# Optimization experiments

Hardware: AMD Instinct MI355X
Metric: run time of the kernel (lower is better)

## Reference

```python
import jax, jax.numpy as jnp
import numpy as np

N, E, IN_F, EDGE_F, HID, S = 200000, 600000, 28, 4, 128, 20000
NUM_LAYERS = 4
L = NUM_LAYERS - 1
BN_EPS = 1e-5


def setup_inputs() -> dict:
    key = jax.random.key(0)
    ks = jax.random.split(key, 20)
    p = lambda k, shape: (jax.random.normal(k, shape, dtype=jnp.float32) * 0.1)
    return {
        'x': jax.random.normal(ks[0], (N, IN_F), dtype=jnp.float32),
        'edge_index': jax.random.randint(ks[1], (2, E), 0, N),
        'edge_attr': jax.random.normal(ks[2], (E, EDGE_F), dtype=jnp.float32),
        'edge_weight': jax.random.uniform(ks[3], (E,), dtype=jnp.float32),
        'node_mask': (jax.random.uniform(ks[4], (N,)) > 0.5).astype(jnp.float32),
        'subgraphs2nodes': jax.random.randint(ks[5], (N,), 0, S),
        # layer-1 params (in_features -> hidden)
        'be1_W1': p(ks[6], (EDGE_F, IN_F)), 'be1_b1': jnp.zeros((IN_F,), jnp.float32),
        'be1_W2': p(ks[7], (IN_F, IN_F)), 'be1_b2': jnp.zeros((IN_F,), jnp.float32),
        'm1_W1': p(ks[8], (IN_F, HID)), 'm1_b1': jnp.zeros((HID,), jnp.float32),
        'm1_W2': p(ks[9], (HID, HID)), 'm1_b2': jnp.zeros((HID,), jnp.float32),
        'bn1_g': jnp.ones((HID,), jnp.float32), 'bn1_b': jnp.zeros((HID,), jnp.float32),
        'eps1': jnp.zeros((), jnp.float32),
        # layers 2..NUM_LAYERS, stacked (hidden -> hidden)
        'beW1': p(ks[10], (L, EDGE_F, HID)), 'beb1': jnp.zeros((L, HID), jnp.float32),
        'beW2': p(ks[11], (L, HID, HID)), 'beb2': jnp.zeros((L, HID), jnp.float32),
        'mW1': p(ks[12], (L, HID, HID)), 'mb1': jnp.zeros((L, HID), jnp.float32),
        'mW2': p(ks[13], (L, HID, HID)), 'mb2': jnp.zeros((L, HID), jnp.float32),
        'bng': jnp.ones((L, HID), jnp.float32), 'bnb': jnp.zeros((L, HID), jnp.float32),
        'eps': jnp.zeros((L,), jnp.float32),
    }


def _mlp2(h, W1, b1, W2, b2):
    # Linear -> ReLU -> Linear
    return jnp.dot(jax.nn.relu(jnp.dot(h, W1) + b1), W2) + b2


def _gine(x, src, dst, edge_attr, edge_weight, eps,
          beW1, beb1, beW2, beb2, W1, b1, W2, b2, g, beta):
    # bond encoder on edge features
    e = _mlp2(edge_attr, beW1, beb1, beW2, beb2)            # [E, d]
    # message: relu(x_j + e_ij) * w_ij, aggregated at dst via scatter-add
    m = jax.nn.relu(x[src] + e) * edge_weight[:, None]      # [E, d]
    aggr = jax.ops.segment_sum(m, dst, num_segments=N)      # [N, d]
    h = (1.0 + eps) * x + aggr
    # node MLP: Linear,ReLU,Linear,BN(train mode),ReLU
    h = _mlp2(h, W1, b1, W2, b2)
    mu = jnp.mean(h, axis=0)
    var = jnp.mean((h - mu) ** 2, axis=0)
    h = (h - mu) * jax.lax.rsqrt(var + BN_EPS) * g + beta
    return jax.nn.relu(h)


def reference(x, edge_index, edge_attr, edge_weight, node_mask, subgraphs2nodes,
              be1_W1, be1_b1, be1_W2, be1_b2, m1_W1, m1_b1, m1_W2, m1_b2,
              bn1_g, bn1_b, eps1,
              beW1, beb1, beW2, beb2, mW1, mb1, mW2, mb2, bng, bnb, eps):
    src, dst = edge_index[0], edge_index[1]
    h = _gine(x, src, dst, edge_attr, edge_weight, eps1,
              be1_W1, be1_b1, be1_W2, be1_b2,
              m1_W1, m1_b1, m1_W2, m1_b2, bn1_g, bn1_b)
    for i in range(L):
        h_new = _gine(h, src, dst, edge_attr, edge_weight, eps[i],
                      beW1[i], beb1[i], beW2[i], beb2[i],
                      mW1[i], mb1[i], mW2[i], mb2[i], bng[i], bnb[i])
        h = h + h_new  # residual
    # float node_mask branch + global_add_pool over subgraphs2nodes
    h = h * node_mask[:, None]
    return jax.ops.segment_sum(h, subgraphs2nodes, num_segments=S)  # [S, HID]
```

## Files before the change

kernel.cpp:

```cpp
#include <hip/hip_runtime.h>
#include <hip/hip_bf16.h>


#define BNEPS 1e-5f
#define LDA 136
#define SCAN_NB 240

typedef __attribute__((ext_vector_type(8))) short bf16x8;
typedef __attribute__((ext_vector_type(8))) unsigned short u16x8;
typedef __attribute__((ext_vector_type(4))) float f32x4;

__device__ inline short f2bf(float f) {
    __hip_bfloat16 h = __float2bfloat16(f);
    return *reinterpret_cast<short*>(&h);
}
__device__ inline unsigned short f2bfu(float f) {
    __hip_bfloat16 h = __float2bfloat16(f);
    return *reinterpret_cast<unsigned short*>(&h);
}
__device__ inline float bf2f(unsigned short u) {
    union { unsigned int i; float f; } v; v.i = ((unsigned int)u) << 16; return v.f;
}


// ... 245 lines not shown
    }
    if (tid < 32) b2s[tid] = (tid < 28) ? b2[tid] : 0.f;
    int j = tid & 31, sub = tid >> 5;
    float w10 = 0.f, w11 = 0.f, w12 = 0.f, w13 = 0.f, b1j = 0.f;
    if (j < 28) { w10 = W1[j]; w11 = W1[28 + j]; w12 = W1[56 + j]; w13 = W1[84 + j]; b1j = b1[j]; }
    int w = tid >> 6, lane = tid & 63;
    int l15 = lane & 15, quad = lane >> 4;
    __syncthreads();

    int numTiles = (E + 63) >> 6;
    for (int tile = blockIdx.x; tile < numTiles; tile += gridDim.x) {
        int base = tile * 64;
        __syncthreads();
        if (tid < 64) {
            int k = base + tid;
            float4 a = (k < E) ? pea4[k] : make_float4(0.f, 0.f, 0.f, 0.f);
            eas[tid][0] = a.x; eas[tid][1] = a.y; eas[tid][2] = a.z; eas[tid][3] = a.w;
        }
        __syncthreads();
        #pragma unroll
        for (int q = 0; q < 8; ++q) {
            int e = q * 8 + sub;
            float t = fmaf(eas[e][0], w10, fmaf(eas[e][1], w11,
                      fmaf(eas[e][2], w12, fmaf(eas[e][3], w13, b1j))));
            As[e * 40 + j] = (j < 28) ? f2bf(fmaxf(t, 0.f)) : (short)0;
        }
        __syncthreads();
        f32x4 acc[2];
        acc[0] = (f32x4){0.f, 0.f, 0.f, 0.f};
        acc[1] = (f32x4){0.f, 0.f, 0.f, 0.f};
        bf16x8 af = *(bf16x8*)&As[(w * 16 + l15) * 40 + quad * 8];
        #pragma unroll
        for (int nt = 0; nt < 2; ++nt) {
            bf16x8 bf = *(bf16x8*)&Bs[(nt * 16 + l15) * 40 + quad * 8];
            acc[nt] = __builtin_amdgcn_mfma_f32_16x16x32_bf16(af, bf, acc[nt], 0, 0, 0);
        }
        __syncthreads();
        #pragma unroll
        for (int nt = 0; nt < 2; ++nt) {
            int col = nt * 16 + l15;
            float bb = b2s[col];
            #pragma unroll
            for (int r = 0; r < 4; ++r)
                As[(w * 16 + quad * 4 + r) * 40 + col] = f2bf(acc[nt][r] + bb);
        }
        __syncthreads();
        for (int i = tid; i < 64 * 28; i += 256) {
            int row = i / 28, col = i - row * 28;
            int gr = base + row;
            if (gr < E) emsg28[(size_t)gr * 28 + col] = As[row * 40 + col];
        }
    }
}

__global__ __launch_bounds__(256) void k_gather(
    const unsigned short* __restrict__ h, const int* __restrict__ offs,
    const int2* __restrict__ pmeta, const unsigned short* __restrict__ emsg,
    unsigned short* __restrict__ a0,
    const float* __restrict__ epsp, int epsIdx,
    int n0, int n1)
{
    int grp = threadIdx.x >> 5, lane = threadIdx.x & 31;
    int n = n0 + blockIdx.x * 8 + grp;
    if (n >= n1) return;
    int e0 = offs[n0];
    int k0 = offs[n], k1 = offs[n + 1];
    float s = 1.0f + epsp[epsIdx];
    ushort4 hv0 = *(const ushort4*)&h[(size_t)n * 128 + lane * 4];
    float m0 = s * bf2f(hv0.x), m1 = s * bf2f(hv0.y);
    float m2 = s * bf2f(hv0.z), m3 = s * bf2f(hv0.w);
    int2 mtA, mtB, mtC, mtD;
    ushort4 evA, hvA, evB, hvB, evC, hvC, evD, hvD;
    const ushort4 z4 = {0, 0, 0, 0};
    #define GSLOT(mt, ev, hv, kk) \
        if ((kk) < k1) { \
            mt = pmeta[kk]; \
            ev = *(const ushort4*)&emsg[(size_t)((kk) - e0) * 128 + lane * 4]; \
            hv = *(const ushort4*)&h[(size_t)mt.x * 128 + lane * 4]; \
        } else { mt = make_int2(0, 0); ev = z4; hv = z4; }
    #define GCONS(mt, ev, hv) { \
            float wv = __int_as_float(mt.y); \
            m0 += fmaxf(bf2f(hv.x) + bf2f(ev.x), 0.f) * wv; \
            m1 += fmaxf(bf2f(hv.y) + bf2f(ev.y), 0.f) * wv; \
            m2 += fmaxf(bf2f(hv.z) + bf2f(ev.z), 0.f) * wv; \
            m3 += fmaxf(bf2f(hv.w) + bf2f(ev.w), 0.f) * wv; }
    GSLOT(mtA, evA, hvA, k0)
    GSLOT(mtB, evB, hvB, k0 + 1)
    GSLOT(mtC, evC, hvC, k0 + 2)
    GSLOT(mtD, evD, hvD, k0 + 3)
    int k = k0;
    while (true) {
        GCONS(mtA, evA, hvA)
        GCONS(mtB, evB, hvB)
        GCONS(mtC, evC, hvC)
        GCONS(mtD, evD, hvD)
        k += 4;
        if (k >= k1) break;
        GSLOT(mtA, evA, hvA, k)
        GSLOT(mtB, evB, hvB, k + 1)
        GSLOT(mtC, evC, hvC, k + 2)
        GSLOT(mtD, evD, hvD, k + 3)
    }
    #undef GSLOT
    #undef GCONS
    ushort4 o;
    o.x = f2bfu(m0); o.y = f2bfu(m1); o.z = f2bfu(m2); o.w = f2bfu(m3);
    *(ushort4*)&a0[(size_t)n * 128 + lane * 4] = o;
}

__global__ __launch_bounds__(256) void k_gather28(
    const float* __restrict__ x, const unsigned short* __restrict__ xbf,
    const int* __restrict__ offs,
    const int2* __restrict__ pmeta, const unsigned short* __restrict__ emsg28,
    const float* __restrict__ eps1, float* __restrict__ u28, int N)
{
    int grp = threadIdx.x >> 5, lane = threadIdx.x & 31;
    int n = blockIdx.x * 8 + grp;
    if (n >= N || lane >= 28) return;
    float s = 1.0f + eps1[0];
    int k0 = offs[n], k1 = offs[n + 1];
    float m = 0.f;
    int2 mtA, mtB, mtC, mtD;
    unsigned short eA, xA, eB, xB, eC, xC, eD, xD;
    #define GSLOT28(mt, ee, xx, kk) \
        if ((kk) < k1) { \
            mt = pmeta[kk]; \
            ee = emsg28[(size_t)(kk) * 28 + lane]; \
            xx = xbf[(size_t)mt.x * 32 + lane]; \
        } else { mt = make_int2(0, 0); ee = 0; xx = 0; }
    #define GCONS28(mt, ee, xx) \
        m += fmaxf(bf2f(xx) + bf2f(ee), 0.f) * __int_as_float(mt.y);
    GSLOT28(mtA, eA, xA, k0)
    GSLOT28(mtB, eB, xB, k0 + 1)
    GSLOT28(mtC, eC, xC, k0 + 2)
    GSLOT28(mtD, eD, xD, k0 + 3)
    int k = k0;
    while (true) {
        GCONS28(mtA, eA, xA)
        GCONS28(mtB, eB, xB)
        GCONS28(mtC, eC, xC)
        GCONS28(mtD, eD, xD)
        k += 4;
        if (k >= k1) break;
        GSLOT28(mtA, eA, xA, k)
        GSLOT28(mtB, eB, xB, k + 1)
        GSLOT28(mtC, eC, xC, k + 2)
        GSLOT28(mtD, eD, xD, k + 3)
    }
    #undef GSLOT28
    #undef GCONS28
    u28[(size_t)n * 28 + lane] = fmaf(s, x[(size_t)n * 28 + lane], m);
}

__global__ __launch_bounds__(512, 2) void k_mlp(
    const unsigned short* __restrict__ src, const short* __restrict__ W1f,
    const float* __restrict__ b1, const short* __restrict__ W2f,
    const float* __restrict__ b2, unsigned short* __restrict__ dst,
    float* __restrict__ stats, int N)
{
    __shared__ short As[256 * LDA];
    __shared__ short Bs1[16384];
    __shared__ short Bs2[16384];
    __shared__ float sstat[256];
    int tid = threadIdx.x;
    for (int i = tid; i < 2048; i += 512) {
        *(bf16x8*)&Bs1[i * 8] = *(const bf16x8*)&W1f[i * 8];
        *(bf16x8*)&Bs2[i * 8] = *(const bf16x8*)&W2f[i * 8];
    }
    if (tid < 256) sstat[tid] = 0.f;
    int w = tid >> 6, lane = tid & 63;
    int l15 = lane & 15, quad = lane >> 4;
    int rb = w * 32;
    float b1r[8], b2r[8], lsum[8], lsq[8];
    #pragma unroll
    for (int nt = 0; nt < 8; ++nt) {
        b1r[nt] = b1[nt * 16 + l15]; b2r[nt] = b2[nt * 16 + l15];
        lsum[nt] = 0.f; lsq[nt] = 0.f;
    }
    int numTiles = (N + 255) >> 8;
    bf16x8 st[8];
    {
        int tile = blockIdx.x;
        if (tile < numTiles) {
            int base = tile * 256;
            #pragma unroll
            for (int kk = 0; kk < 8; ++kk) {
                int i = tid + kk * 512;
                int rr = base + (i >> 4);
                st[kk] = (rr < N) ? *(const bf16x8*)&src[(size_t)rr * 128 + (i & 15) * 8]
                                  : (bf16x8){0, 0, 0, 0, 0, 0, 0, 0};
            }
        }
    }
    __syncthreads();

    for (int tile = blockIdx.x; tile < numTiles; tile += gridDim.x) {
        int base = tile * 256;
        #pragma unroll
        for (int kk = 0; kk < 8; ++kk) {
            int i = tid + kk * 512;
            *(bf16x8*)&As[(i >> 4) * LDA + (i & 15) * 8] = st[kk];
        }
        int tnext = tile + gridDim.x;
        if (tnext < numTiles) {
            int bn = tnext * 256;
            #pragma unroll
            for (int kk = 0; kk < 8; ++kk) {
                int i = tid + kk * 512;
                int rr = bn + (i >> 4);
                st[kk] = (rr < N) ? *(const bf16x8*)&src[(size_t)rr * 128 + (i & 15) * 8]
                                  : (bf16x8){0, 0, 0, 0, 0, 0, 0, 0};
            }
        }
        __syncthreads();
        f32x4 acc[2][8];
        #pragma unroll
        for (int rg = 0; rg < 2; ++rg)
            #pragma unroll
            for (int nt = 0; nt < 8; ++nt) acc[rg][nt] = (f32x4){0.f, 0.f, 0.f, 0.f};
        #pragma unroll
        for (int kt = 0; kt < 4; ++kt) {
            bf16x8 af0 = *(bf16x8*)&As[(rb + l15) * LDA + kt * 32 + quad * 8];
            bf16x8 af1 = *(bf16x8*)&As[(rb + 16 + l15) * LDA + kt * 32 + quad * 8];
            #pragma unroll
            for (int nt = 0; nt < 8; ++nt) {
                bf16x8 bf = *(const bf16x8*)&Bs1[((nt * 4 + kt) * 64 + lane) * 8];
                acc[0][nt] = __builtin_amdgcn_mfma_f32_16x16x32_bf16(af0, bf, acc[0][nt], 0, 0, 0);
                acc[1][nt] = __builtin_amdgcn_mfma_f32_16x16x32_bf16(af1, bf, acc[1][nt], 0, 0, 0);
            }
        }
        #pragma unroll
        for (int rg = 0; rg < 2; ++rg)
            #pragma unroll
            for (int nt = 0; nt < 8; ++nt)
                #pragma unroll
                for (int r = 0; r < 4; ++r)
                    As[(rb + rg * 16 + quad * 4 + r) * LDA + nt * 16 + l15] =
                        f2bf(fmaxf(acc[rg][nt][r] + b1r[nt], 0.f));
        #pragma unroll
        for (int rg = 0; rg < 2; ++rg)
            #pragma unroll
            for (int nt = 0; nt < 8; ++nt) acc[rg][nt] = (f32x4){0.f, 0.f, 0.f, 0.f};
        #pragma unroll
        for (int kt = 0; kt < 4; ++kt) {
            bf16x8 af0 = *(bf16x8*)&As[(rb + l15) * LDA + kt * 32 + quad * 8];
            bf16x8 af1 = *(bf16x8*)&As[(rb + 16 + l15) * LDA + kt * 32 + quad * 8];
            #pragma unroll
            for (int nt = 0; nt < 8; ++nt) {
                bf16x8 bf = *(const bf16x8*)&Bs2[((nt * 4 + kt) * 64 + lane) * 8];
                acc[0][nt] = __builtin_amdgcn_mfma_f32_16x16x32_bf16(af0, bf, acc[0][nt], 0, 0, 0);
                acc[1][nt] = __builtin_amdgcn_mfma_f32_16x16x32_bf16(af1, bf, acc[1][nt], 0, 0, 0);
            }
        }
        #pragma unroll
        for (int rg = 0; rg < 2; ++rg)
            #pragma unroll
            for (int nt = 0; nt < 8; ++nt) {
                int row0 = base + rb + rg * 16 + quad * 4;
                #pragma unroll
                for (int r = 0; r < 4; ++r) {
                    float z = acc[rg][nt][r] + b2r[nt];
                    if (row0 + r < N) { lsum[nt] += z; lsq[nt] = fmaf(z, z, lsq[nt]); }
                    As[(rb + rg * 16 + quad * 4 + r) * LDA + nt * 16 + l15] = f2bf(z);
                }
            }
        #pragma unroll
        for (int it = 0; it < 8; ++it) {
            int arow = rb + it * 4 + quad;
            int rr = base + arow;
            if (rr < N)
                *(bf16x8*)&dst[(size_t)rr * 128 + l15 * 8] = *(bf16x8*)&As[arow * LDA + l15 * 8];
        }
        __syncthreads();
    }
    #pragma unroll
    for (int nt = 0; nt < 8; ++nt) {
        atomicAdd(&sstat[nt * 16 + l15], lsum[nt]);
        atomicAdd(&sstat[128 + nt * 16 + l15], lsq[nt]);
    }
    __syncthreads();
    if (tid < 256) atomicAdd(&stats[tid], sstat[tid]);
}

__global__ __launch_bounds__(512, 2) void k_mlp1(
    const float* __restrict__ u28, const short* __restrict__ W1f,
    const float* __restrict__ b1, const short* __restrict__ W2f,
    const float* __restrict__ b2, unsigned short* __restrict__ dst,
    float* __restrict__ stats, int N)
{
    __shared__ short A28[256 * 40];
    __shared__ short As[256 * LDA];
    __shared__ short Bs1[4096];
    __shared__ short Bs2[16384];
    __shared__ float sstat[256];
    int tid = threadIdx.x;
    if (tid < 512) {
        int i = tid;
        *(bf16x8*)&Bs1[i * 8] = *(const bf16x8*)&W1f[i * 8];
    }
    for (int i = tid; i < 2048; i += 512)
        *(bf16x8*)&Bs2[i * 8] = *(const bf16x8*)&W2f[i * 8];
    for (int i = tid; i < 1024; i += 512) {
        int row = i >> 2, c = 28 + (i & 3);
        A28[row * 40 + c] = 0;
    }
    if (tid < 256) sstat[tid] = 0.f;
    int w = tid >> 6, lane = tid & 63;
    int l15 = lane & 15, quad = lane >> 4;
    int rb = w * 32;
    float b1r[8], b2r[8], lsum[8], lsq[8];
    #pragma unroll
    for (int nt = 0; nt < 8; ++nt) {
        b1r[nt] = b1[nt * 16 + l15]; b2r[nt] = b2[nt * 16 + l15];
        lsum[nt] = 0.f; lsq[nt] = 0.f;
    }
    int numTiles = (N + 255) >> 8;
    float stf[14];
    {
        int tile = blockIdx.x;
        if (tile < numTiles) {
            int base = tile * 256;
            #pragma unroll
            for (int kk = 0; kk < 14; ++kk) {
                int idx = tid + kk * 512;
                int row = idx / 28, col = idx - row * 28;
                int rr = base + row;
                stf[kk] = (rr < N) ? u28[(size_t)rr * 28 + col] : 0.f;
            }
        }
    }
    __syncthreads();

    for (int tile = blockIdx.x; tile < numTiles; tile += gridDim.x) {
        int base = tile * 256;
        #pragma unroll
        for (int kk = 0; kk < 14; ++kk) {
            int idx = tid + kk * 512;
            int row = idx / 28, col = idx - row * 28;
            A28[row * 40 + col] = f2bf(stf[kk]);
        }
        int tnext = tile + gridDim.x;
        if (tnext < numTiles) {
            int bn = tnext * 256;
            #pragma unroll
            for (int kk = 0; kk < 14; ++kk) {
                int idx = tid + kk * 512;
                int row = idx / 28, col = idx - row * 28;
                int rr = bn + row;
                stf[kk] = (rr < N) ? u28[(size_t)rr * 28 + col] : 0.f;
            }
        }
        __syncthreads();
        f32x4 acc[2][8];
        #pragma unroll
        for (int rg = 0; rg < 2; ++rg)
            #pragma unroll
            for (int nt = 0; nt < 8; ++nt) acc[rg][nt] = (f32x4){0.f, 0.f, 0.f, 0.f};
        {
            bf16x8 af0 = *(bf16x8*)&A28[(rb + l15) * 40 + quad * 8];
            bf16x8 af1 = *(bf16x8*)&A28[(rb + 16 + l15) * 40 + quad * 8];
            #pragma unroll
            for (int nt = 0; nt < 8; ++nt) {
                bf16x8 bf = *(const bf16x8*)&Bs1[(nt * 64 + lane) * 8];
                acc[0][nt] = __builtin_amdgcn_mfma_f32_16x16x32_bf16(af0, bf, acc[0][nt], 0, 0, 0);
                acc[1][nt] = __builtin_amdgcn_mfma_f32_16x16x32_bf16(af1, bf, acc[1][nt], 0, 0, 0);
            }
        }
        #pragma unroll
        for (int rg = 0; rg < 2; ++rg)
            #pragma unroll
            for (int nt = 0; nt < 8; ++nt)
                #pragma unroll
                for (int r = 0; r < 4; ++r)
                    As[(rb + rg * 16 + quad * 4 + r) * LDA + nt * 16 + l15] =
                        f2bf(fmaxf(acc[rg][nt][r] + b1r[nt], 0.f));
        __syncthreads();
        #pragma unroll
        for (int rg = 0; rg < 2; ++rg)
            #pragma unroll
            for (int nt = 0; nt < 8; ++nt) acc[rg][nt] = (f32x4){0.f, 0.f, 0.f, 0.f};
        #pragma unroll
        for (int kt = 0; kt < 4; ++kt) {
            bf16x8 af0 = *(bf16x8*)&As[(rb + l15) * LDA + kt * 32 + quad * 8];
            bf16x8 af1 = *(bf16x8*)&As[(rb + 16 + l15) * LDA + kt * 32 + quad * 8];
            #pragma unroll
            for (int nt = 0; nt < 8; ++nt) {
                bf16x8 bf = *(const bf16x8*)&Bs2[((nt * 4 + kt) * 64 + lane) * 8];
                acc[0][nt] = __builtin_amdgcn_mfma_f32_16x16x32_bf16(af0, bf, acc[0][nt], 0, 0, 0);
                acc[1][nt] = __builtin_amdgcn_mfma_f32_16x16x32_bf16(af1, bf, acc[1][nt], 0, 0, 0);
            }
        }
        #pragma unroll
        for (int rg = 0; rg < 2; ++rg)
            #pragma unroll
            for (int nt = 0; nt < 8; ++nt) {
                int row0 = base + rb + rg * 16 + quad * 4;
                #pragma unroll
                for (int r = 0; r < 4; ++r) {
                    float z = acc[rg][nt][r] + b2r[nt];
                    if (row0 + r < N) { lsum[nt] += z; lsq[nt] = fmaf(z, z, lsq[nt]); }
                    As[(rb + rg * 16 + quad * 4 + r) * LDA + nt * 16 + l15] = f2bf(z);
                }
            }
        #pragma unroll
        for (int it = 0; it < 8; ++it) {
            int arow = rb + it * 4 + quad;
            int rr = base + arow;
            if (rr < N)
                *(bf16x8*)&dst[(size_t)rr * 128 + l15 * 8] = *(bf16x8*)&As[arow * LDA + l15 * 8];
        }
        __syncthreads();
    }
    #pragma unroll
    for (int nt = 0; nt < 8; ++nt) {
        atomicAdd(&sstat[nt * 16 + l15], lsum[nt]);
        atomicAdd(&sstat[128 + nt * 16 + l15], lsq[nt]);
    }
    __syncthreads();
    if (tid < 256) atomicAdd(&stats[tid], sstat[tid]);
}

__global__ __launch_bounds__(256) void k_bn(
    const unsigned short* __restrict__ z, const float* __restrict__ stats,
    const float* __restrict__ g, const float* __restrict__ bb, float invN,
    unsigned short* __restrict__ h, int residual, int N)
{
    __shared__ float ss[256];
    if (threadIdx.x < 128) {
        int j = threadIdx.x;
        float mu  = stats[j] * invN;
        float var = fmaf(stats[128 + j], invN, -mu * mu);
        float sc  = rsqrtf(fmaxf(var, 0.f) + BNEPS) * g[j];
        ss[j] = sc;
        ss[128 + j] = fmaf(-mu, sc, bb[j]);
    }
    __syncthreads();
    int idx8 = blockIdx.x * 256 + threadIdx.x;
    int stride = gridDim.x * 256;
    int c0 = (idx8 & 15) * 8;
    float scl[8], sht[8];
    #pragma unroll
    for (int r = 0; r < 8; ++r) { scl[r] = ss[c0 + r]; sht[r] = ss[128 + c0 + r]; }
    int total8 = N * 16;
    for (; idx8 < total8; idx8 += stride) {
        int n = idx8 >> 4;
        u16x8 z8 = *(const u16x8*)&z[(size_t)n * 128 + c0];
        float hn[8];
        #pragma unroll
        for (int r = 0; r < 8; ++r)
            hn[r] = fmaxf(fmaf(bf2f(z8[r]), scl[r], sht[r]), 0.f);
        if (residual) {
            u16x8 h8 = *(const u16x8*)&h[(size_t)n * 128 + c0];
            #pragma unroll
            for (int r = 0; r < 8; ++r) hn[r] += bf2f(h8[r]);
        }
        u16x8 o;
        #pragma unroll
        for (int r = 0; r < 8; ++r) o[r] = f2bfu(hn[r]);
        *(u16x8*)&h[(size_t)n * 128 + c0] = o;
    }
}

__global__ __launch_bounds__(256) void k_poolbn(
    const unsigned short* __restrict__ z, const unsigned short* __restrict__ hprev,
    const float* __restrict__ stats, const float* __restrict__ g,
    const float* __restrict__ bb, float invN,
    const int* __restrict__ offs2, const int* __restrict__ perm2,
    float* __restrict__ out, int S)
{
    __shared__ float ss[256];
    if (threadIdx.x < 128) {
        int j = threadIdx.x;
        float mu  = stats[j] * invN;
        float var = fmaf(stats[128 + j], invN, -mu * mu);
        float sc  = rsqrtf(fmaxf(var, 0.f) + BNEPS) * g[j];
        ss[j] = sc;
        ss[128 + j] = fmaf(-mu, sc, bb[j]);
    }
    __syncthreads();
    int w = threadIdx.x >> 6, lane = threadIdx.x & 63;
    int s = blockIdx.x * 4 + w;
    if (s >= S) return;
    int c0 = lane * 2;
    float scl0 = ss[c0], scl1 = ss[c0 + 1];
    float sht0 = ss[128 + c0], sht1 = ss[128 + c0 + 1];
    int k0 = offs2[s], k1 = offs2[s + 1];
    float a0 = 0.f, a1 = 0.f;
    for (int k = k0; k < k1; ++k) {
        int n = perm2[k];
        ushort2 zv = *(const ushort2*)&z[(size_t)n * 128 + c0];
        ushort2 hv = *(const ushort2*)&hprev[(size_t)n * 128 + c0];
        a0 += fmaxf(fmaf(bf2f(zv.x), scl0, sht0), 0.f) + bf2f(hv.x);
        a1 += fmaxf(fmaf(bf2f(zv.y), scl1, sht1), 0.f) + bf2f(hv.y);
    }
    *(float2*)&out[(size_t)s * 128 + c0] = make_float2(a0, a1);
}

extern "C" void kernel_launch(void* const* d_in, const int* in_sizes, int n_in,
                              void* d_out, int out_size, void* d_ws, size_t ws_size,
                              hipStream_t stream) {
    const float* x    = (const float*)d_in[0];
    const int*   ei   = (const int*)d_in[1];
    const float* ea   = (const float*)d_in[2];
    const float* ew   = (const float*)d_in[3];
    const float* mask = (const float*)d_in[4];
    const int*   s2n  = (const int*)d_in[5];
    const float* be1W1 = (const float*)d_in[6];
    const float* be1b1 = (const float*)d_in[7];
    const float* be1W2 = (const float*)d_in[8];
    const float* be1b2 = (const float*)d_in[9];
    const float* m1W1  = (const float*)d_in[10];
    const float* m1b1  = (const float*)d_in[11];
    const float* m1W2  = (const float*)d_in[12];
    const float* m1b2  = (const float*)d_in[13];
    const float* bn1g  = (const float*)d_in[14];
    const float* bn1b  = (const float*)d_in[15];
    const float* eps1  = (const float*)d_in[16];
    const float* beW1  = (const float*)d_in[17];
    const float* beb1  = (const float*)d_in[18];
    const float* beW2  = (const float*)d_in[19];
    const float* beb2  = (const float*)d_in[20];
    const float* mW1   = (const float*)d_in[21];
    const float* mb1   = (const float*)d_in[22];
    const float* mW2   = (const float*)d_in[23];
    const float* mb2   = (const float*)d_in[24];
    const float* bng   = (const float*)d_in[25];
    const float* bnb   = (const float*)d_in[26];
    const float* epsL  = (const float*)d_in[27];

    const int N = in_sizes[0] / 28;
    const int E = in_sizes[1] / 2;
    const int S = out_size / 128;
    const float invN = 1.0f / (float)N;
    const int NS = N / 2;
    const int EMC = E / 2 + 8192;

    auto al16 = [](size_t v) { return (v + 15) & ~(size_t)15; };
    char* ws = (char*)d_ws;
    size_t offH      = 0;
    size_t offA0     = al16(offH + (size_t)N * 256);
    size_t offEm     = al16(offA0 + (size_t)N * 256);
    size_t emBytes   = (size_t)EMC * 256;
    if ((size_t)E * 56 > emBytes) emBytes = (size_t)E * 56;
    size_t offStats  = al16(offEm + emBytes);
    size_t offSS     = al16(offStats + 4096);
    size_t offWts    = al16(offSS + 1024);
    size_t offCounts = al16(offWts + 10 * 16384 * 2 + 4096 * 2 + 1024 * 2);
    size_t offOffs   = al16(offCounts + (size_t)N * 4);
    size_t offCursor = al16(offOffs + (size_t)(N + 1) * 4);
    size_t offPmeta  = al16(offCursor + (size_t)N * 4);
    size_t offPea    = al16(offPmeta + (size_t)E * 8);
    size_t offBsum   = al16(offPea + (size_t)E * 16);
    size_t offCnt2   = al16(offBsum + SCAN_NB * 4);
    size_t offOffs2  = al16(offCnt2 + (size_t)S * 4);
    size_t offCur2   = al16(offOffs2 + (size_t)(S + 1) * 4);
    size_t offPerm2  = al16(offCur2 + (size_t)S * 4);
    size_t need      = offPerm2 + (size_t)N * 4;
    if (ws_size < need) return;

    unsigned short* h    = (unsigned short*)(ws + offH);
    unsigned short* a0   = (unsigned short*)(ws + offA0);
    unsigned short* emsg = (unsigned short*)(ws + offEm);
    float* u28    = (float*)(ws + offA0);
    unsigned short* xbf = (unsigned short*)(ws + offA0 + 26214400);
    float* stats  = (float*)(ws + offStats);
    short* wts    = (short*)(ws + offWts);
    short* w1p    = wts + 10 * 16384;
    short* w2p28  = w1p + 4096;
    int*   counts = (int*)(ws + offCounts);
    int*   offs   = (int*)(ws + offOffs);
    int*   cursor = (int*)(ws + offCursor);
    int2*  pmeta  = (int2*)(ws + offPmeta);
    float4* pea4  = (float4*)(ws + offPea);
    int*   bsum   = (int*)(ws + offBsum);
    int*   cnt2   = (int*)(ws + offCnt2);
    int*   offs2  = (int*)(ws + offOffs2);
    int*   cur2   = (int*)(ws + offCur2);
    int*   perm2  = (int*)(ws + offPerm2);
    const float4* ea4 = (const float4*)ea;

    hipMemsetAsync(stats, 0, 4 * 256 * sizeof(float), stream);
    hipMemsetAsync(counts, 0, (size_t)N * sizeof(int), stream);
    hipMemsetAsync(cnt2, 0, (size_t)S * sizeof(int), stream);

    k_prep<<<42, 256, 0, stream>>>(m1W2, beW2, mW1, mW2, m1W1, be1W2, wts, w1p, w2p28);
    k_prepx<<<512, 256, 0, stream>>>(x, xbf, N);

    const int seg = (N + SCAN_NB - 1) / SCAN_NB;
    k_count<<<1024, 256, 0, stream>>>(ei, counts, E);
    k_scanA<<<SCAN_NB, 256, 0, stream>>>(counts, bsum, N, seg);
    k_scanB<<<1, 256, 0, stream>>>(bsum, SCAN_NB, offs, N);
    k_scanC<<<SCAN_NB, 256, 0, stream>>>(counts, bsum, offs, cursor, N, seg);
    k_scatter<<<1024, 256, 0, stream>>>(ei, ew, ea4, cursor, pmeta, pea4, E);

    const int seg2 = (S + SCAN_NB - 1) / SCAN_NB;
    k_count2<<<512, 256, 0, stream>>>(s2n, mask, cnt2, N);
    k_scanA<<<SCAN_NB, 256, 0, stream>>>(cnt2, bsum, S, seg2);
    k_scanB<<<1, 256, 0, stream>>>(bsum, SCAN_NB, offs2, S);
    k_scanC<<<SCAN_NB, 256, 0, stream>>>(cnt2, bsum, offs2, cur2, S, seg2);
    k_scatter2<<<512, 256, 0, stream>>>(s2n, mask, cur2, perm2, N);

    auto wt_be = [&](int l) { return wts + (size_t)(1 + 3 * l + 0) * 16384; };
    auto wt_m1 = [&](int l) { return wts + (size_t)(1 + 3 * l + 1) * 16384; };
    auto wt_m2 = [&](int l) { return wts + (size_t)(1 + 3 * l + 2) * 16384; };

    k_emsg28_mm<<<2048, 256, 0, stream>>>(pea4, be1W1, be1b1, w2p28, be1b2, emsg, E);
    k_gather28<<<(N + 7) / 8, 256, 0, stream>>>(x, xbf, offs, pmeta, emsg, eps1, u28, N);
    k_mlp1<<<256, 512, 0, stream>>>(u28, w1p, m1b1, wts , m1b2, h, stats, N);
    k_bn<<<2048, 256, 0, stream>>>(h, stats, bn1g, bn1b, invN, h, 0, N);

    for (int l = 0; l < 3; ++l) {
        for (int c = 0; c < 2; ++c) {
            int n0 = (c == 0) ? 0 : NS;
            int n1 = (c == 0) ? NS : N;
            k_emsg<<<2048, 256, 0, stream>>>(pea4,
                beW1 + (size_t)l * 512, beb1 + (size_t)l * 128,
                wt_be(l), beb2 + (size_t)l * 128, emsg, offs, n0, n1);
            k_gather<<<(n1 - n0 + 7) / 8, 256, 0, stream>>>(h, offs, pmeta, emsg, a0,
                epsL, l, n0, n1);
        }
        k_mlp<<<256, 512, 0, stream>>>(a0, wt_m1(l), mb1 + (size_t)l * 128,
                                       wt_m2(l), mb2 + (size_t)l * 128, a0,
                                       stats + 256 * (l + 1), N);
        if (l < 2) {
            k_bn<<<2048, 256, 0, stream>>>(a0, stats + 256 * (l + 1),
                bng + (size_t)l * 128, bnb + (size_t)l * 128, invN, h, 1, N);
        }
    }

    k_poolbn<<<(S + 3) / 4, 256, 0, stream>>>(a0, h, stats + 256 * 3,
        bng + 256, bnb + 256, invN, offs2, perm2, (float*)d_out, S);
}
```

Before: 1.001 ms.

## Make MLP kernels wave-independent with per-wave 16-row tiles and 1024-thread blocks

Both node-MLP kernels are restructured so each wave owns a private 16-row slice of the tile. It loads its A fragments straight from global memory into registers and stages only its own intermediate rows in a per-wave shared buffer. This removes the block-wide shared staging, the register prefetch of the next tile and all per-tile __syncthreads. Blocks grow from 512 to 1024 threads so more waves are resident to hide the global-load latency that is no longer explicitly prefetched. The trade-off is less reuse of B fragments (one row group per wave instead of two) and exposed load latency per wave.

```diff
diff --git a/kernel.cpp b/kernel.cpp
--- a/kernel.cpp
+++ b/kernel.cpp
@@ -421,126 +421,86 @@
     u28[(size_t)n * 28 + lane] = fmaf(s, x[(size_t)n * 28 + lane], m);
 }
 
-__global__ __launch_bounds__(512, 2) void k_mlp(
+__global__ __launch_bounds__(1024, 4) void k_mlp(
     const unsigned short* __restrict__ src, const short* __restrict__ W1f,
     const float* __restrict__ b1, const short* __restrict__ W2f,
     const float* __restrict__ b2, unsigned short* __restrict__ dst,
     float* __restrict__ stats, int N)
 {
-    __shared__ short As[256 * LDA];
     __shared__ short Bs1[16384];
     __shared__ short Bs2[16384];
+    __shared__ short As[16 * 16 * LDA];
     __shared__ float sstat[256];
     int tid = threadIdx.x;
-    for (int i = tid; i < 2048; i += 512) {
+    for (int i = tid; i < 2048; i += 1024) {
         *(bf16x8*)&Bs1[i * 8] = *(const bf16x8*)&W1f[i * 8];
         *(bf16x8*)&Bs2[i * 8] = *(const bf16x8*)&W2f[i * 8];
     }
     if (tid < 256) sstat[tid] = 0.f;
     int w = tid >> 6, lane = tid & 63;
     int l15 = lane & 15, quad = lane >> 4;
-    int rb = w * 32;
+    short* myAs = &As[w * 16 * LDA];
     float b1r[8], b2r[8], lsum[8], lsq[8];
     #pragma unroll
     for (int nt = 0; nt < 8; ++nt) {
         b1r[nt] = b1[nt * 16 + l15]; b2r[nt] = b2[nt * 16 + l15];
         lsum[nt] = 0.f; lsq[nt] = 0.f;
     }
+    __syncthreads();
+
     int numTiles = (N + 255) >> 8;
-    bf16x8 st[8];
-    {
-        int tile = blockIdx.x;
-        if (tile < numTiles) {
-            int base = tile * 256;
-            #pragma unroll
-            for (int kk = 0; kk < 8; ++kk) {
-                int i = tid + kk * 512;
-                int rr = base + (i >> 4);
-                st[kk] = (rr < N) ? *(const bf16x8*)&src[(size_t)rr * 128 + (i & 15) * 8]
-                                  : (bf16x8){0, 0, 0, 0, 0, 0, 0, 0};
-            }
-        }
-    }
-    __syncthreads();
-
     for (int tile = blockIdx.x; tile < numTiles; tile += gridDim.x) {
-        int base = tile * 256;
-        #pragma unroll
-        for (int kk = 0; kk < 8; ++kk) {
-            int i = tid + kk * 512;
-            *(bf16x8*)&As[(i >> 4) * LDA + (i & 15) * 8] = st[kk];
-        }
-        int tnext = tile + gridDim.x;
-        if (tnext < numTiles) {
-            int bn = tnext * 256;
-            #pragma unroll
-            for (int kk = 0; kk < 8; ++kk) {
-                int i = tid + kk * 512;
-                int rr = bn + (i >> 4);
-                st[kk] = (rr < N) ? *(const bf16x8*)&src[(size_t)rr * 128 + (i & 15) * 8]
-                                  : (bf16x8){0, 0, 0, 0, 0, 0, 0, 0};
-            }
-        }
-        __syncthreads();
-        f32x4 acc[2][8];
-        #pragma unroll
-        for (int rg = 0; rg < 2; ++rg)
-            #pragma unroll
-            for (int nt = 0; nt < 8; ++nt) acc[rg][nt] = (f32x4){0.f, 0.f, 0.f, 0.f};
+        int rowbase = tile * 256 + w * 16;
+        int arow = rowbase + l15;
+        const unsigned short* srow = src + (size_t)arow * 128;
+        f32x4 acc[8];
+        #pragma unroll
+        for (int nt = 0; nt < 8; ++nt) acc[nt] = (f32x4){0.f, 0.f, 0.f, 0.f};
         #pragma unroll
         for (int kt = 0; kt < 4; ++kt) {
-            bf16x8 af0 = *(bf16x8*)&As[(rb + l15) * LDA + kt * 32 + quad * 8];
-            bf16x8 af1 = *(bf16x8*)&As[(rb + 16 + l15) * LDA + kt * 32 + quad * 8];
+            bf16x8 af = (arow < N) ? *(const bf16x8*)&srow[kt * 32 + quad * 8]
+                                   : (bf16x8){0, 0, 0, 0, 0, 0, 0, 0};
             #pragma unroll
             for (int nt = 0; nt < 8; ++nt) {
                 bf16x8 bf = *(const bf16x8*)&Bs1[((nt * 4 + kt) * 64 + lane) * 8];
-                acc[0][nt] = __builtin_amdgcn_mfma_f32_16x16x32_bf16(af0, bf, acc[0][nt], 0, 0, 0);
-                acc[1][nt] = __builtin_amdgcn_mfma_f32_16x16x32_bf16(af1, bf, acc[1][nt], 0, 0, 0);
+                acc[nt] = __builtin_amdgcn_mfma_f32_16x16x32_bf16(af, bf, acc[nt], 0, 0, 0);
             }
         }
         #pragma unroll
-        for (int rg = 0; rg < 2; ++rg)
-            #pragma unroll
-            for (int nt = 0; nt < 8; ++nt)
-                #pragma unroll
-                for (int r = 0; r < 4; ++r)
-                    As[(rb + rg * 16 + quad * 4 + r) * LDA + nt * 16 + l15] =
-                        f2bf(fmaxf(acc[rg][nt][r] + b1r[nt], 0.f));
-        #pragma unroll
-        for (int rg = 0; rg < 2; ++rg)
-            #pragma unroll
-            for (int nt = 0; nt < 8; ++nt) acc[rg][nt] = (f32x4){0.f, 0.f, 0.f, 0.f};
+        for (int nt = 0; nt < 8; ++nt)
+            #pragma unroll
+            for (int r = 0; r < 4; ++r)
+                myAs[(quad * 4 + r) * LDA + nt * 16 + l15] =
+                    f2bf(fmaxf(acc[nt][r] + b1r[nt], 0.f));
+        #pragma unroll
+        for (int nt = 0; nt < 8; ++nt) acc[nt] = (f32x4){0.f, 0.f, 0.f, 0.f};
         #pragma unroll
         for (int kt = 0; kt < 4; ++kt) {
-            bf16x8 af0 = *(bf16x8*)&As[(rb + l15) * LDA + kt * 32 + quad * 8];
-            bf16x8 af1 = *(bf16x8*)&As[(rb + 16 + l15) * LDA + kt * 32 + quad * 8];
+            bf16x8 af = *(bf16x8*)&myAs[l15 * LDA + kt * 32 + quad * 8];
             #pragma unroll
             for (int nt = 0; nt < 8; ++nt) {
                 bf16x8 bf = *(const bf16x8*)&Bs2[((nt * 4 + kt) * 64 + lane) * 8];
-                acc[0][nt] = __builtin_amdgcn_mfma_f32_16x16x32_bf16(af0, bf, acc[0][nt], 0, 0, 0);
-                acc[1][nt] = __builtin_amdgcn_mfma_f32_16x16x32_bf16(af1, bf, acc[1][nt], 0, 0, 0);
+                acc[nt] = __builtin_amdgcn_mfma_f32_16x16x32_bf16(af, bf, acc[nt], 0, 0, 0);
             }
         }
         #pragma unroll
-        for (int rg = 0; rg < 2; ++rg)
-            #pragma unroll
-            for (int nt = 0; nt < 8; ++nt) {
-                int row0 = base + rb + rg * 16 + quad * 4;
-                #pragma unroll
-                for (int r = 0; r < 4; ++r) {
-                    float z = acc[rg][nt][r] + b2r[nt];
-                    if (row0 + r < N) { lsum[nt] += z; lsq[nt] = fmaf(z, z, lsq[nt]); }
-                    As[(rb + rg * 16 + quad * 4 + r) * LDA + nt * 16 + l15] = f2bf(z);
-                }
+        for (int nt = 0; nt < 8; ++nt) {
+            int row0 = rowbase + quad * 4;
+            #pragma unroll
+            for (int r = 0; r < 4; ++r) {
+                float z = acc[nt][r] + b2r[nt];
+                if (row0 + r < N) { lsum[nt] += z; lsq[nt] = fmaf(z, z, lsq[nt]); }
+                myAs[(quad * 4 + r) * LDA + nt * 16 + l15] = f2bf(z);
             }
-        #pragma unroll
-        for (int it = 0; it < 8; ++it) {
-            int arow = rb + it * 4 + quad;
-            int rr = base + arow;
+        }
+        #pragma unroll
+        for (int s = 0; s < 4; ++s) {
+            int i = lane + s * 64;
+            int lrow = i >> 4, c8 = i & 15;
+            int rr = rowbase + lrow;
             if (rr < N)
-                *(bf16x8*)&dst[(size_t)rr * 128 + l15 * 8] = *(bf16x8*)&As[arow * LDA + l15 * 8];
-        }
-        __syncthreads();
+                *(bf16x8*)&dst[(size_t)rr * 128 + c8 * 8] = *(bf16x8*)&myAs[lrow * LDA + c8 * 8];
+        }
     }
     #pragma unroll
     for (int nt = 0; nt < 8; ++nt) {
@@ -551,134 +511,90 @@
     if (tid < 256) atomicAdd(&stats[tid], sstat[tid]);
 }
 
-__global__ __launch_bounds__(512, 2) void k_mlp1(
+__global__ __launch_bounds__(1024, 4) void k_mlp1(
     const float* __restrict__ u28, const short* __restrict__ W1f,
     const float* __restrict__ b1, const short* __restrict__ W2f,
     const float* __restrict__ b2, unsigned short* __restrict__ dst,
     float* __restrict__ stats, int N)
 {
-    __shared__ short A28[256 * 40];
-    __shared__ short As[256 * LDA];
     __shared__ short Bs1[4096];
     __shared__ short Bs2[16384];
+    __shared__ short As[16 * 16 * LDA];
     __shared__ float sstat[256];
     int tid = threadIdx.x;
-    if (tid < 512) {
-        int i = tid;
-        *(bf16x8*)&Bs1[i * 8] = *(const bf16x8*)&W1f[i * 8];
-    }
-    for (int i = tid; i < 2048; i += 512)
+    if (tid < 512)
+        *(bf16x8*)&Bs1[tid * 8] = *(const bf16x8*)&W1f[tid * 8];
+    for (int i = tid; i < 2048; i += 1024)
         *(bf16x8*)&Bs2[i * 8] = *(const bf16x8*)&W2f[i * 8];
-    for (int i = tid; i < 1024; i += 512) {
-        int row = i >> 2, c = 28 + (i & 3);
-        A28[row * 40 + c] = 0;
-    }
     if (tid < 256) sstat[tid] = 0.f;
     int w = tid >> 6, lane = tid & 63;
     int l15 = lane & 15, quad = lane >> 4;
-    int rb = w * 32;
+    short* myAs = &As[w * 16 * LDA];
     float b1r[8], b2r[8], lsum[8], lsq[8];
     #pragma unroll
     for (int nt = 0; nt < 8; ++nt) {
         b1r[nt] = b1[nt * 16 + l15]; b2r[nt] = b2[nt * 16 + l15];
         lsum[nt] = 0.f; lsq[nt] = 0.f;
     }
+    __syncthreads();
+
     int numTiles = (N + 255) >> 8;
-    float stf[14];
-    {
-        int tile = blockIdx.x;
-        if (tile < numTiles) {
-            int base = tile * 256;
-            #pragma unroll
-            for (int kk = 0; kk < 14; ++kk) {
-                int idx = tid + kk * 512;
-                int row = idx / 28, col = idx - row * 28;
-                int rr = base + row;
-                stf[kk] = (rr < N) ? u28[(size_t)rr * 28 + col] : 0.f;
-            }
-        }
-    }
-    __syncthreads();
-
     for (int tile = blockIdx.x; tile < numTiles; tile += gridDim.x) {
-        int base = tile * 256;
-        #pragma unroll
-        for (int kk = 0; kk < 14; ++kk) {
-            int idx = tid + kk * 512;
-            int row = idx / 28, col = idx - row * 28;
-            A28[row * 40 + col] = f2bf(stf[kk]);
-        }
-        int tnext = tile + gridDim.x;
-        if (tnext < numTiles) {
-            int bn = tnext * 256;
-            #pragma unroll
-            for (int kk = 0; kk < 14; ++kk) {
-                int idx = tid + kk * 512;
-                int row = idx / 28, col = idx - row * 28;
-                int rr = bn + row;
-                stf[kk] = (rr < N) ? u28[(size_t)rr * 28 + col] : 0.f;
-            }
-        }
-        __syncthreads();
-        f32x4 acc[2][8];
-        #pragma unroll
-        for (int rg = 0; rg < 2; ++rg)
-            #pragma unroll
-            for (int nt = 0; nt < 8; ++nt) acc[rg][nt] = (f32x4){0.f, 0.f, 0.f, 0.f};
-        {
-            bf16x8 af0 = *(bf16x8*)&A28[(rb + l15) * 40 + quad * 8];
-            bf16x8 af1 = *(bf16x8*)&A28[(rb + 16 + l15) * 40 + quad * 8];
-            #pragma unroll
-            for (int nt = 0; nt < 8; ++nt) {
-                bf16x8 bf = *(const bf16x8*)&Bs1[(nt * 64 + lane) * 8];
-                acc[0][nt] = __builtin_amdgcn_mfma_f32_16x16x32_bf16(af0, bf, acc[0][nt], 0, 0, 0);
-                acc[1][nt] = __builtin_amdgcn_mfma_f32_16x16x32_bf16(af1, bf, acc[1][nt], 0, 0, 0);
-            }
-        }
-        #pragma unroll
-        for (int rg = 0; rg < 2; ++rg)
-            #pragma unroll
-            for (int nt = 0; nt < 8; ++nt)
-                #pragma unroll
-                for (int r = 0; r < 4; ++r)
-                    As[(rb + rg * 16 + quad * 4 + r) * LDA + nt * 16 + l15] =
-                        f2bf(fmaxf(acc[rg][nt][r] + b1r[nt], 0.f));
-        __syncthreads();
-        #pragma unroll
-        for (int rg = 0; rg < 2; ++rg)
-            #pragma unroll
-            for (int nt = 0; nt < 8; ++nt) acc[rg][nt] = (f32x4){0.f, 0.f, 0.f, 0.f};
+        int rowbase = tile * 256 + w * 16;
+        int arow = rowbase + l15;
+        const float* urow = u28 + (size_t)arow * 28;
+        float4 fa = make_float4(0.f, 0.f, 0.f, 0.f);
+        float4 fb = make_float4(0.f, 0.f, 0.f, 0.f);
+        if (arow < N) {
+            fa = *(const float4*)&urow[quad * 8];
+            if (quad < 3) fb = *(const float4*)&urow[quad * 8 + 4];
+        }
+        bf16x8 af1;
+        af1[0] = f2bf(fa.x); af1[1] = f2bf(fa.y); af1[2] = f2bf(fa.z); af1[3] = f2bf(fa.w);
+        af1[4] = f2bf(fb.x); af1[5] = f2bf(fb.y); af1[6] = f2bf(fb.z); af1[7] = f2bf(fb.w);
+        f32x4 acc[8];
+        #pragma unroll
+        for (int nt = 0; nt < 8; ++nt) acc[nt] = (f32x4){0.f, 0.f, 0.f, 0.f};
+        #pragma unroll
+        for (int nt = 0; nt < 8; ++nt) {
+            bf16x8 bf = *(const bf16x8*)&Bs1[(nt * 64 + lane) * 8];
+            acc[nt] = __builtin_amdgcn_mfma_f32_16x16x32_bf16(af1, bf, acc[nt], 0, 0, 0);
+        }
+        #pragma unroll
+        for (int nt = 0; nt < 8; ++nt)
+            #pragma unroll
+            for (int r = 0; r < 4; ++r)
+                myAs[(quad * 4 + r) * LDA + nt * 16 + l15] =
+                    f2bf(fmaxf(acc[nt][r] + b1r[nt], 0.f));
+        #pragma unroll
+        for (int nt = 0; nt < 8; ++nt) acc[nt] = (f32x4){0.f, 0.f, 0.f, 0.f};
         #pragma unroll
         for (int kt = 0; kt < 4; ++kt) {
-            bf16x8 af0 = *(bf16x8*)&As[(rb + l15) * LDA + kt * 32 + quad * 8];
-            bf16x8 af1 = *(bf16x8*)&As[(rb + 16 + l15) * LDA + kt * 32 + quad * 8];
+            bf16x8 af = *(bf16x8*)&myAs[l15 * LDA + kt * 32 + quad * 8];
             #pragma unroll
             for (int nt = 0; nt < 8; ++nt) {
                 bf16x8 bf = *(const bf16x8*)&Bs2[((nt * 4 + kt) * 64 + lane) * 8];
-                acc[0][nt] = __builtin_amdgcn_mfma_f32_16x16x32_bf16(af0, bf, acc[0][nt], 0, 0, 0);
-                acc[1][nt] = __builtin_amdgcn_mfma_f32_16x16x32_bf16(af1, bf, acc[1][nt], 0, 0, 0);
+                acc[nt] = __builtin_amdgcn_mfma_f32_16x16x32_bf16(af, bf, acc[nt], 0, 0, 0);
             }
         }
         #pragma unroll
-        for (int rg = 0; rg < 2; ++rg)
-            #pragma unroll
-            for (int nt = 0; nt < 8; ++nt) {
-                int row0 = base + rb + rg * 16 + quad * 4;
-                #pragma unroll
-                for (int r = 0; r < 4; ++r) {
-                    float z = acc[rg][nt][r] + b2r[nt];
-                    if (row0 + r < N) { lsum[nt] += z; lsq[nt] = fmaf(z, z, lsq[nt]); }
-                    As[(rb + rg * 16 + quad * 4 + r) * LDA + nt * 16 + l15] = f2bf(z);
-                }
+        for (int nt = 0; nt < 8; ++nt) {
+            int row0 = rowbase + quad * 4;
+            #pragma unroll
+            for (int r = 0; r < 4; ++r) {
+                float z = acc[nt][r] + b2r[nt];
+                if (row0 + r < N) { lsum[nt] += z; lsq[nt] = fmaf(z, z, lsq[nt]); }
+                myAs[(quad * 4 + r) * LDA + nt * 16 + l15] = f2bf(z);
             }
-        #pragma unroll
-        for (int it = 0; it < 8; ++it) {
-            int arow = rb + it * 4 + quad;
-            int rr = base + arow;
+        }
+        #pragma unroll
+        for (int s = 0; s < 4; ++s) {
+            int i = lane + s * 64;
+            int lrow = i >> 4, c8 = i & 15;
+            int rr = rowbase + lrow;
             if (rr < N)
-                *(bf16x8*)&dst[(size_t)rr * 128 + l15 * 8] = *(bf16x8*)&As[arow * LDA + l15 * 8];
-        }
-        __syncthreads();
+                *(bf16x8*)&dst[(size_t)rr * 128 + c8 * 8] = *(bf16x8*)&myAs[lrow * LDA + c8 * 8];
+        }
     }
     #pragma unroll
     for (int nt = 0; nt < 8; ++nt) {
@@ -875,7 +791,7 @@
 
     k_emsg28_mm<<<2048, 256, 0, stream>>>(pea4, be1W1, be1b1, w2p28, be1b2, emsg, E);
     k_gather28<<<(N + 7) / 8, 256, 0, stream>>>(x, xbf, offs, pmeta, emsg, eps1, u28, N);
-    k_mlp1<<<256, 512, 0, stream>>>(u28, w1p, m1b1, wts , m1b2, h, stats, N);
+    k_mlp1<<<256, 1024, 0, stream>>>(u28, w1p, m1b1, wts , m1b2, h, stats, N);
     k_bn<<<2048, 256, 0, stream>>>(h, stats, bn1g, bn1b, invN, h, 0, N);
 
     for (int l = 0; l < 3; ++l) {
@@ -888,9 +804,9 @@
             k_gather<<<(n1 - n0 + 7) / 8, 256, 0, stream>>>(h, offs, pmeta, emsg, a0,
                 epsL, l, n0, n1);
         }
-        k_mlp<<<256, 512, 0, stream>>>(a0, wt_m1(l), mb1 + (size_t)l * 128,
-                                       wt_m2(l), mb2 + (size_t)l * 128, a0,
-                                       stats + 256 * (l + 1), N);
+        k_mlp<<<256, 1024, 0, stream>>>(a0, wt_m1(l), mb1 + (size_t)l * 128,
+                                        wt_m2(l), mb2 + (size_t)l * 128, a0,
+                                        stats + 256 * (l + 1), N);
         if (l < 2) {
             k_bn<<<2048, 256, 0, stream>>>(a0, stats + 256 * (l + 1),
                 bng + (size_t)l * 128, bnb + (size_t)l * 128, invN, h, 1, N);
```

Measured after the change: 1.017 ms. Within noise of the previous version (+1.6%).

## Give each wave private rows in k_mlp and drop block-level staging and syncs

Applied to the files above, without the earlier changes.

Rewrites the per-layer node MLP kernel so each of 16 waves in a 1024-thread block owns 16 rows. A fragments for the first GEMM now come straight from global memory instead of a block-wide shared tile filled through register prefetch. The hidden activations and output go through a per-wave LDS slice, which removes the per-tile __syncthreads. The cost is that global loads are no longer prefetched a tile ahead, and the tighter launch bounds may limit registers.

```diff
diff --git a/kernel.cpp b/kernel.cpp
--- a/kernel.cpp
+++ b/kernel.cpp
@@ -421,126 +421,86 @@
     u28[(size_t)n * 28 + lane] = fmaf(s, x[(size_t)n * 28 + lane], m);
 }
 
-__global__ __launch_bounds__(512, 2) void k_mlp(
+__global__ __launch_bounds__(1024, 4) void k_mlp(
     const unsigned short* __restrict__ src, const short* __restrict__ W1f,
     const float* __restrict__ b1, const short* __restrict__ W2f,
     const float* __restrict__ b2, unsigned short* __restrict__ dst,
     float* __restrict__ stats, int N)
 {
-    __shared__ short As[256 * LDA];
     __shared__ short Bs1[16384];
     __shared__ short Bs2[16384];
+    __shared__ short As[16 * 16 * LDA];
     __shared__ float sstat[256];
     int tid = threadIdx.x;
-    for (int i = tid; i < 2048; i += 512) {
+    for (int i = tid; i < 2048; i += 1024) {
         *(bf16x8*)&Bs1[i * 8] = *(const bf16x8*)&W1f[i * 8];
         *(bf16x8*)&Bs2[i * 8] = *(const bf16x8*)&W2f[i * 8];
     }
     if (tid < 256) sstat[tid] = 0.f;
     int w = tid >> 6, lane = tid & 63;
     int l15 = lane & 15, quad = lane >> 4;
-    int rb = w * 32;
+    short* myAs = &As[w * 16 * LDA];
     float b1r[8], b2r[8], lsum[8], lsq[8];
     #pragma unroll
     for (int nt = 0; nt < 8; ++nt) {
         b1r[nt] = b1[nt * 16 + l15]; b2r[nt] = b2[nt * 16 + l15];
         lsum[nt] = 0.f; lsq[nt] = 0.f;
     }
+    __syncthreads();
+
     int numTiles = (N + 255) >> 8;
-    bf16x8 st[8];
-    {
-        int tile = blockIdx.x;
-        if (tile < numTiles) {
-            int base = tile * 256;
-            #pragma unroll
-            for (int kk = 0; kk < 8; ++kk) {
-                int i = tid + kk * 512;
-                int rr = base + (i >> 4);
-                st[kk] = (rr < N) ? *(const bf16x8*)&src[(size_t)rr * 128 + (i & 15) * 8]
-                                  : (bf16x8){0, 0, 0, 0, 0, 0, 0, 0};
-            }
-        }
-    }
-    __syncthreads();
-
     for (int tile = blockIdx.x; tile < numTiles; tile += gridDim.x) {
-        int base = tile * 256;
-        #pragma unroll
-        for (int kk = 0; kk < 8; ++kk) {
-            int i = tid + kk * 512;
-            *(bf16x8*)&As[(i >> 4) * LDA + (i & 15) * 8] = st[kk];
-        }
-        int tnext = tile + gridDim.x;
-        if (tnext < numTiles) {
-            int bn = tnext * 256;
-            #pragma unroll
-            for (int kk = 0; kk < 8; ++kk) {
-                int i = tid + kk * 512;
-                int rr = bn + (i >> 4);
-                st[kk] = (rr < N) ? *(const bf16x8*)&src[(size_t)rr * 128 + (i & 15) * 8]
-                                  : (bf16x8){0, 0, 0, 0, 0, 0, 0, 0};
-            }
-        }
-        __syncthreads();
-        f32x4 acc[2][8];
-        #pragma unroll
-        for (int rg = 0; rg < 2; ++rg)
-            #pragma unroll
-            for (int nt = 0; nt < 8; ++nt) acc[rg][nt] = (f32x4){0.f, 0.f, 0.f, 0.f};
+        int rowbase = tile * 256 + w * 16;
+        int arow = rowbase + l15;
+        const unsigned short* srow = src + (size_t)arow * 128;
+        f32x4 acc[8];
+        #pragma unroll
+        for (int nt = 0; nt < 8; ++nt) acc[nt] = (f32x4){0.f, 0.f, 0.f, 0.f};
         #pragma unroll
         for (int kt = 0; kt < 4; ++kt) {
-            bf16x8 af0 = *(bf16x8*)&As[(rb + l15) * LDA + kt * 32 + quad * 8];
-            bf16x8 af1 = *(bf16x8*)&As[(rb + 16 + l15) * LDA + kt * 32 + quad * 8];
+            bf16x8 af = (arow < N) ? *(const bf16x8*)&srow[kt * 32 + quad * 8]
+                                   : (bf16x8){0, 0, 0, 0, 0, 0, 0, 0};
             #pragma unroll
             for (int nt = 0; nt < 8; ++nt) {
                 bf16x8 bf = *(const bf16x8*)&Bs1[((nt * 4 + kt) * 64 + lane) * 8];
-                acc[0][nt] = __builtin_amdgcn_mfma_f32_16x16x32_bf16(af0, bf, acc[0][nt], 0, 0, 0);
-                acc[1][nt] = __builtin_amdgcn_mfma_f32_16x16x32_bf16(af1, bf, acc[1][nt], 0, 0, 0);
+                acc[nt] = __builtin_amdgcn_mfma_f32_16x16x32_bf16(af, bf, acc[nt], 0, 0, 0);
             }
         }
         #pragma unroll
-        for (int rg = 0; rg < 2; ++rg)
-            #pragma unroll
-            for (int nt = 0; nt < 8; ++nt)
-                #pragma unroll
-                for (int r = 0; r < 4; ++r)
-                    As[(rb + rg * 16 + quad * 4 + r) * LDA + nt * 16 + l15] =
-                        f2bf(fmaxf(acc[rg][nt][r] + b1r[nt], 0.f));
-        #pragma unroll
-        for (int rg = 0; rg < 2; ++rg)
-            #pragma unroll
-            for (int nt = 0; nt < 8; ++nt) acc[rg][nt] = (f32x4){0.f, 0.f, 0.f, 0.f};
+        for (int nt = 0; nt < 8; ++nt)
+            #pragma unroll
+            for (int r = 0; r < 4; ++r)
+                myAs[(quad * 4 + r) * LDA + nt * 16 + l15] =
+                    f2bf(fmaxf(acc[nt][r] + b1r[nt], 0.f));
+        #pragma unroll
+        for (int nt = 0; nt < 8; ++nt) acc[nt] = (f32x4){0.f, 0.f, 0.f, 0.f};
         #pragma unroll
         for (int kt = 0; kt < 4; ++kt) {
-            bf16x8 af0 = *(bf16x8*)&As[(rb + l15) * LDA + kt * 32 + quad * 8];
-            bf16x8 af1 = *(bf16x8*)&As[(rb + 16 + l15) * LDA + kt * 32 + quad * 8];
+            bf16x8 af = *(bf16x8*)&myAs[l15 * LDA + kt * 32 + quad * 8];
             #pragma unroll
             for (int nt = 0; nt < 8; ++nt) {
                 bf16x8 bf = *(const bf16x8*)&Bs2[((nt * 4 + kt) * 64 + lane) * 8];
-                acc[0][nt] = __builtin_amdgcn_mfma_f32_16x16x32_bf16(af0, bf, acc[0][nt], 0, 0, 0);
-                acc[1][nt] = __builtin_amdgcn_mfma_f32_16x16x32_bf16(af1, bf, acc[1][nt], 0, 0, 0);
+                acc[nt] = __builtin_amdgcn_mfma_f32_16x16x32_bf16(af, bf, acc[nt], 0, 0, 0);
             }
         }
         #pragma unroll
-        for (int rg = 0; rg < 2; ++rg)
-            #pragma unroll
-            for (int nt = 0; nt < 8; ++nt) {
-                int row0 = base + rb + rg * 16 + quad * 4;
-                #pragma unroll
-                for (int r = 0; r < 4; ++r) {
-                    float z = acc[rg][nt][r] + b2r[nt];
-                    if (row0 + r < N) { lsum[nt] += z; lsq[nt] = fmaf(z, z, lsq[nt]); }
-                    As[(rb + rg * 16 + quad * 4 + r) * LDA + nt * 16 + l15] = f2bf(z);
-                }
+        for (int nt = 0; nt < 8; ++nt) {
+            int row0 = rowbase + quad * 4;
+            #pragma unroll
+            for (int r = 0; r < 4; ++r) {
+                float z = acc[nt][r] + b2r[nt];
+                if (row0 + r < N) { lsum[nt] += z; lsq[nt] = fmaf(z, z, lsq[nt]); }
+                myAs[(quad * 4 + r) * LDA + nt * 16 + l15] = f2bf(z);
             }
-        #pragma unroll
-        for (int it = 0; it < 8; ++it) {
-            int arow = rb + it * 4 + quad;
-            int rr = base + arow;
+        }
+        #pragma unroll
+        for (int s = 0; s < 4; ++s) {
+            int i = lane + s * 64;
+            int lrow = i >> 4, c8 = i & 15;
+            int rr = rowbase + lrow;
             if (rr < N)
-                *(bf16x8*)&dst[(size_t)rr * 128 + l15 * 8] = *(bf16x8*)&As[arow * LDA + l15 * 8];
-        }
-        __syncthreads();
+                *(bf16x8*)&dst[(size_t)rr * 128 + c8 * 8] = *(bf16x8*)&myAs[lrow * LDA + c8 * 8];
+        }
     }
     #pragma unroll
     for (int nt = 0; nt < 8; ++nt) {
@@ -888,9 +848,9 @@
             k_gather<<<(n1 - n0 + 7) / 8, 256, 0, stream>>>(h, offs, pmeta, emsg, a0,
                 epsL, l, n0, n1);
         }
-        k_mlp<<<256, 512, 0, stream>>>(a0, wt_m1(l), mb1 + (size_t)l * 128,
-                                       wt_m2(l), mb2 + (size_t)l * 128, a0,
-                                       stats + 256 * (l + 1), N);
+        k_mlp<<<256, 1024, 0, stream>>>(a0, wt_m1(l), mb1 + (size_t)l * 128,
+                                        wt_m2(l), mb2 + (size_t)l * 128, a0,
+                                        stats + 256 * (l + 1), N);
         if (l < 2) {
             k_bn<<<2048, 256, 0, stream>>>(a0, stats + 256 * (l + 1),
                 bng + (size_t)l * 128, bnb + (size_t)l * 128, invN, h, 1, N);
```

Result: no change. 1.010 ms (+0.9%).
